# Optimization experiments

Measured on AMD Instinct MI355X. Metric: run time of the kernel, lower is better.

## Reference

```python
import jax, jax.numpy as jnp
import numpy as np

N = 50000   # nodes (= node_input)
H = 128     # node_hidden
E = 800000  # edges per adjacency


def spmm(row, col, val, dense):
    # (sparse NxN) @ dense[N, F] via gather + segment_sum
    return jax.ops.segment_sum(dense[col] * val[:, None], row, num_segments=N)


def l2norm(x, eps=1e-12):
    n = jnp.sqrt(jnp.sum(x * x, axis=1, keepdims=True))
    return x / jnp.maximum(n, eps)


def setup_inputs() -> dict:
    key = jax.random.key(0)
    ks = jax.random.split(key, 20)
    stdv = 1.0 / np.sqrt(H)
    u = lambda k, shape, s: jax.random.uniform(k, shape, jnp.float32, -s, s)
    inp = {
        'in_row': jax.random.randint(ks[0], (E,), 0, N),
        'in_col': jax.random.randint(ks[1], (E,), 0, N),
        'in_val': jax.random.uniform(ks[2], (E,), jnp.float32),
        'out_row': jax.random.randint(ks[3], (E,), 0, N),
        'out_col': jax.random.randint(ks[4], (E,), 0, N),
        'out_val': jax.random.uniform(ks[5], (E,), jnp.float32),
        'W1': u(ks[6], (N, H), stdv), 'b1': u(ks[7], (H,), stdv),
        'W2': u(ks[8], (H, H), stdv), 'b2': u(ks[9], (H,), stdv),
        'W3': u(ks[10], (H, H), stdv), 'b3': u(ks[11], (H,), stdv),
        'W4': u(ks[12], (H, H), stdv), 'b4': u(ks[13], (H,), stdv),
        'lin1_w': jax.random.normal(ks[14], (2 * H, H), jnp.float32) * 0.05,
        'lin1_b': jnp.zeros((2 * H,), jnp.float32),
        'lin2_w': jax.random.normal(ks[15], (2 * H, 2 * H), jnp.float32) * 0.05,
        'lin2_b': jnp.zeros((2 * H,), jnp.float32),
        'lin3_w': jax.random.normal(ks[16], (1, 2 * H), jnp.float32) * 0.05,
        'lin3_b': jnp.zeros((1,), jnp.float32),
    }
    return inp


def reference(in_row, in_col, in_val, out_row, out_col, out_val,
              W1, b1, W2, b2, W3, b3, W4, b4,
              lin1_w, lin1_b, lin2_w, lin2_b, lin3_w, lin3_b):
    def branch(row, col, val):
        x1 = l2norm(jax.nn.relu(spmm(row, col, val, W1) + b1))
        x2 = l2norm(jax.nn.relu(spmm(row, col, val, x1 @ W2) + b2))
        x3 = l2norm(jax.nn.relu(spmm(row, col, val, x2 @ W3) + b3))
        x4 = jax.nn.relu(spmm(row, col, val, x3 @ W4) + b4)
        return (x1, x2, x3, x4)

    def score(x):  # dropout p=0.0 -> identity
        h = jax.nn.relu(x @ lin1_w.T + lin1_b)
        h = jax.nn.relu(h @ lin2_w.T + lin2_b)
        return h @ lin3_w.T + lin3_b

    xs_in = branch(in_row, in_col, in_val)
    xs_out = branch(out_row, out_col, out_val)
    score_in = sum(score(x) for x in xs_in)
    score_out = sum(score(x) for x in xs_out)
    return score_in * score_out
```

## Files before the change

### kernel.cpp

```cpp
#include <hip/hip_runtime.h>
#include <hip/hip_bf16.h>

#define NN 50000
#define HH 128
#define H2 256
#define EE 800000
#define NBUCK 196
#define BINCH 4096
#define QB 128

typedef _Float16 half8 __attribute__((ext_vector_type(8)));
typedef float float4v __attribute__((ext_vector_type(4)));

__device__ __forceinline__ float bf2f(unsigned short u) {
  union { unsigned int i; float f; } v; v.i = ((unsigned int)u) << 16; return v.f;
}
__device__ __forceinline__ unsigned short f2bf(float f) {
  union { float f; unsigned int i; } v; v.f = f;
  unsigned int x = v.i;
  unsigned int r = x + 0x7fffu + ((x >> 16) & 1u);
  return (unsigned short)(r >> 16);
}

__device__ __forceinline__ unsigned int uenc(float x) {
  unsigned int b = (unsigned int)(x * 255.f + 0.5f);
  return b > 255u ? 255u : b;
}

__device__ __forceinline__ void udec(unsigned int wd, float vs, float* a) {
  a[0] = fmaf(vs, (float)(wd & 0xffu), a[0]);
  a[1] = fmaf(vs, (float)((wd >> 8) & 0xffu), a[1]);
  a[2] = fmaf(vs, (float)((wd >> 16) & 0xffu), a[2]);
  a[3] = fmaf(vs, (float)(wd >> 24), a[3]);
}

__global__ void detect_kernel(const unsigned int* __restrict__ val, int* __restrict__ dt) {
  unsigned int w = val[threadIdx.x];
  unsigned short u = (unsigned short)(w & 0xffff);
  int expf = (u >> 7) & 0xff;
  bool match = ((u >> 15) == 0) && expf >= 0x5A && expf <= 0x7E;
  unsigned long long m = __ballot(match);
  if (threadIdx.x == 0) dt[0] = (__popcll(m) >= 48) ? 1 : 0;
}

#define NSEG 14
struct ConvSegs {
  const void* s[NSEG];
  void* d[NSEG];
  int n[NSEG];
  int mode[NSEG];
  int kd[NSEG];
  int bstart[NSEG + 1];
};

__global__ __launch_bounds__(256) void convall_kernel(ConvSegs cs, const int* __restrict__ dt) {
  int b = blockIdx.x;
  int seg = 0;
  while (b >= cs.bstart[seg + 1]) ++seg;
  int i = (b - cs.bstart[seg]) * 256 + threadIdx.x;
  if (i >= cs.n[seg]) return;
  float f = dt[0] ? bf2f(((const unsigned short*)cs.s[seg])[i])
                  : ((const float*)cs.s[seg])[i];
  int m = cs.mode[seg];
  if (m == 0) { ((float*)cs.d[seg])[i] = f; return; }
  if (m == 1) { ((_Float16*)cs.d[seg])[i] = (_Float16)f; return; }
  int K = cs.kd[seg];
  int n, k;
  if (m == 3) { n = i / K; k = i - n * K; }
  else        { k = i >> 7; n = i & 127; }
  int NC16 = (cs.n[seg] / K) >> 4;
  int off = ((k >> 5) * NC16 + (n >> 4)) * 512 + (((k >> 3) & 3) * 16 + (n & 15)) * 8 + (k & 7);
  ((_Float16*)cs.d[seg])[off] = (_Float16)f;
}

__global__ __launch_bounds__(256) void bincount_kernel(
    const int* __restrict__ r0, const int* __restrict__ r1,
    int* __restrict__ bcnt, int E) {
  int br = blockIdx.y;
  const int* rows = br ? r1 : r0;
  __shared__ int cnt_s[NBUCK];
  int t = threadIdx.x;
  for (int i = t; i < NBUCK; i += 256) cnt_s[i] = 0;
  __syncthreads();
  int e0 = blockIdx.x * BINCH;
  #pragma unroll
  for (int i = 0; i < 16; ++i) {
    int e = e0 + i * 256 + t;
    if (e < E) atomicAdd(&cnt_s[rows[e] >> 8], 1);
  }
  __syncthreads();
  for (int i = t; i < NBUCK; i += 256) {
    int c = cnt_s[i];
    if (c) atomicAdd(&bcnt[br * NBUCK + i], c);
  }
}

__global__ __launch_bounds__(256) void bscan_kernel(const int* __restrict__ bcnt,
                                                    int* __restrict__ bbase,
                                                    int* __restrict__ gcur) {
  int br = blockIdx.y, t = threadIdx.x;
  __shared__ int s[256];
  int v = (t < NBUCK) ? bcnt[br * NBUCK + t] : 0;
  s[t] = v;
  __syncthreads();
  for (int off = 1; off < 256; off <<= 1) {
    int u = (t >= off) ? s[t - off] : 0;
    __syncthreads();
    s[t] += u;
    __syncthreads();
  }
  int ex = s[t] - v;
  if (t < NBUCK) { bbase[br * NBUCK + t] = ex; gcur[br * NBUCK + t] = ex; }
}

__global__ __launch_bounds__(256) void bin_kernel(
    const int* __restrict__ r0, const int* __restrict__ r1,
    const int* __restrict__ c0, const int* __restrict__ c1,
    const void* __restrict__ v0, const void* __restrict__ v1,
    int* __restrict__ gcur, int2* __restrict__ binned, int E, const int* __restrict__ dt) {
  int br = blockIdx.y;
  const int* rows = br ? r1 : r0;
  const int* cols = br ? c1 : c0;
  const void* vals = br ? v1 : v0;
  int2* bout = binned + (size_t)br * EE;
  int* cur = gcur + br * NBUCK;
  __shared__ int cnt_s[NBUCK];
  __shared__ int base_s[NBUCK];
  int t = threadIdx.x;
  for (int i = t; i < NBUCK; i += 256) cnt_s[i] = 0;
  __syncthreads();
  int e0 = blockIdx.x * BINCH;
  int row[16], col[16], vb[16];
  int cnt = 0;
  bool isb = dt[0] != 0;
  #pragma unroll
  for (int i = 0; i < 16; ++i) {
    int e = e0 + i * 256 + t;
    if (e < E) {
      row[cnt] = rows[e];
      col[cnt] = cols[e];
      float v = isb ? bf2f(((const unsigned short*)vals)[e]) : ((const float*)vals)[e];
      vb[cnt] = __float_as_int(v);
      atomicAdd(&cnt_s[row[cnt] >> 8], 1);
      ++cnt;
    }
  }
  __syncthreads();
  for (int i = t; i < NBUCK; i += 256) {
    int c = cnt_s[i];
    base_s[i] = c ? atomicAdd(&cur[i], c) : 0;
    cnt_s[i] = 0;
  }
  __syncthreads();
  for (int i = 0; i < cnt; ++i) {
    int b = row[i] >> 8;
    int off = atomicAdd(&cnt_s[b], 1);
    bout[base_s[b] + off] = make_int2((row[i] << 16) | col[i], vb[i]);
  }
}

__global__ __launch_bounds__(256) void bucket_kernel(
    const int* __restrict__ bbase, const int2* __restrict__ binned,
    int2* __restrict__ edges, int* __restrict__ rp, int N, int E) {
  int br = blockIdx.y, b = blockIdx.x, t = threadIdx.x;
  const int2* bin = binned + (size_t)br * EE;
  int2* eo = edges + (size_t)br * EE;
  int* r = rp + br * (NN + 1);
  __shared__ int cur[256];
  __shared__ int s[256];
  int base = bbase[br * NBUCK + b];
  int end  = (b + 1 < NBUCK) ? bbase[br * NBUCK + b + 1] : E;
  cur[t] = 0;
  __syncthreads();
  for (int i = base + t; i < end; i += 256)
    atomicAdd(&cur[(((unsigned)bin[i].x) >> 16) & 255], 1);
  __syncthreads();
  int v = cur[t];
  s[t] = v;
  __syncthreads();
  for (int off = 1; off < 256; off <<= 1) {
    int u = (t >= off) ? s[t - off] : 0;
    __syncthreads();
    s[t] += u;
    __syncthreads();
  }
  int ex = base + s[t] - v;
  int row = b * 256 + t;
  if (row < N) r[row] = ex;
  if (b == 0 && t == 0) r[N] = E;
  cur[t] = ex;
  __syncthreads();
  for (int i = base + t; i < end; i += 256) {
    int2 e = bin[i];
    int rl = (((unsigned)e.x) >> 16) & 255;
    int p = atomicAdd(&cur[rl], 1);
    eo[p] = make_int2(e.x & 0xffff, e.y);
  }
}

template<int DO_L2, int SQ>
__global__ __launch_bounds__(256) void spmm_kernel(
    const int* __restrict__ rp, const int2* __restrict__ edges,
    const _Float16* __restrict__ src, size_t sstride, const float* __restrict__ bias,
    _Float16* __restrict__ dst, size_t dstride, unsigned char* __restrict__ dstq, int N)
{
  const size_t XQC = (size_t)(NN + 128) * QB;
  int br = blockIdx.y;
  rp += br * (NN + 1);
  edges += (size_t)br * EE;
  src += br * sstride;
  dst += br * dstride;
  if (SQ) dstq += br * XQC;
  int g = threadIdx.x >> 4;
  int l = threadIdx.x & 15;
  int r = blockIdx.x * 16 + g;
  if (r >= N) return;
  int kb = rp[r], ke = rp[r + 1];
  float a0[8] = {0,0,0,0,0,0,0,0}, a1[8] = {0,0,0,0,0,0,0,0};
  float a2[8] = {0,0,0,0,0,0,0,0}, a3[8] = {0,0,0,0,0,0,0,0};
  int k = kb;
  for (; k + 3 < ke; k += 4) {
    int2 e0 = edges[k], e1 = edges[k + 1], e2 = edges[k + 2], e3 = edges[k + 3];
    half8 s0 = *(const half8*)(src + (size_t)e0.x * HH + l * 8);
    half8 s1 = *(const half8*)(src + (size_t)e1.x * HH + l * 8);
    half8 s2 = *(const half8*)(src + (size_t)e2.x * HH + l * 8);
    half8 s3 = *(const half8*)(src + (size_t)e3.x * HH + l * 8);
    float v0 = __int_as_float(e0.y), v1 = __int_as_float(e1.y);
    float v2 = __int_as_float(e2.y), v3 = __int_as_float(e3.y);
    #pragma unroll
    for (int j = 0; j < 8; ++j) {
      a0[j] = fmaf(v0, (float)s0[j], a0[j]);
      a1[j] = fmaf(v1, (float)s1[j], a1[j]);
      a2[j] = fmaf(v2, (float)s2[j], a2[j]);
      a3[j] = fmaf(v3, (float)s3[j], a3[j]);
    }
  }
  for (; k < ke; ++k) {
    int2 e0 = edges[k];
    half8 s0 = *(const half8*)(src + (size_t)e0.x * HH + l * 8);
    float v0 = __int_as_float(e0.y);
    #pragma unroll
    for (int j = 0; j < 8; ++j) a0[j] = fmaf(v0, (float)s0[j], a0[j]);
  }
  float x[8];
  #pragma unroll
  for (int j = 0; j < 8; ++j)
    x[j] = fmaxf((a0[j] + a1[j]) + (a2[j] + a3[j]) + bias[l * 8 + j], 0.f);
  if (DO_L2) {
    float ss = 0.f;
    #pragma unroll
    for (int j = 0; j < 8; ++j) ss += x[j] * x[j];
    #pragma unroll
    for (int m = 1; m < 16; m <<= 1) ss += __shfl_xor(ss, m, 64);
    float sc = 1.f / fmaxf(sqrtf(ss), 1e-12f);
    #pragma unroll
    for (int j = 0; j < 8; ++j) x[j] *= sc;
  }
  half8 hv;
  #pragma unroll
  for (int j = 0; j < 8; ++j) hv[j] = (_Float16)x[j];
  *(half8*)&dst[(size_t)r * HH + l * 8] = hv;
  if (SQ) {
    uint2 qo;
    qo.x = uenc(x[0]) | (uenc(x[1]) << 8) | (uenc(x[2]) << 16) | (uenc(x[3]) << 24);
    qo.y = uenc(x[4]) | (uenc(x[5]) << 8) | (uenc(x[6]) << 16) | (uenc(x[7]) << 24);
    *(uint2*)(dstq + (size_t)r * QB + l * 8) = qo;
  }
}

template<int DO_L2, int GQ, int SQ>
__global__ __launch_bounds__(256, 6) void fused_kernel(
    const int* __restrict__ rp, const int2* __restrict__ edges,
    const _Float16* __restrict__ xcur, const unsigned char* __restrict__ xq,
    _Float16* __restrict__ xnext, unsigned char* __restrict__ xnq,
    const _Float16* __restrict__ wt, const float* __restrict__ bias,
    const _Float16* __restrict__ w1, const _Float16* __restrict__ w2,
    const float* __restrict__ b1v, const float* __restrict__ b2v,
    const float* __restrict__ w3v,
    float* __restrict__ S, int N, int sg, int gx, int nsp)
{
  extern __shared__ _Float16 smem[];
  const size_t XSC = (size_t)(NN + 128) * HH;
  const size_t XQC = (size_t)(NN + 128) * QB;
  int br = blockIdx.y;
  rp += br * (NN + 1);
  edges += (size_t)br * EE;
  xcur += br * XSC;
  if (GQ) xq += br * XQC;

  int bx = blockIdx.x;
  int role, idx;
  if (nsp) {
    int q = bx / 3, k3 = bx - q * 3;
    if (k3 < 2) { idx = q * 2 + k3; if (idx >= sg) return; role = 0; }
    else        { idx = q;          if (idx >= gx) return; role = 1; }
  } else { role = 1; idx = bx; if (idx >= gx) return; }

  const int lane = threadIdx.x & 63, w = threadIdx.x >> 6;
  const int lm = lane & 15, lq = lane >> 4;

  if (role == 0) {
    xnext += br * XSC;
    if (SQ) xnq += br * XQC;
    int g = threadIdx.x >> 4, l = threadIdx.x & 15;
    int r = idx * 16 + g;
    int kb = rp[r], ke = rp[r + 1];
    half8 hv;
    float a0[8] = {0,0,0,0,0,0,0,0}, a1[8] = {0,0,0,0,0,0,0,0};
    float a2[8] = {0,0,0,0,0,0,0,0}, a3[8] = {0,0,0,0,0,0,0,0};
    if (GQ) {
      int k = kb;
      for (; k + 3 < ke; k += 4) {
        int2 e0 = edges[k], e1 = edges[k + 1], e2 = edges[k + 2], e3 = edges[k + 3];
        uint2 q0 = *(const uint2*)(xq + (size_t)e0.x * QB + l * 8);
        uint2 q1 = *(const uint2*)(xq + (size_t)e1.x * QB + l * 8);
        uint2 q2 = *(const uint2*)(xq + (size_t)e2.x * QB + l * 8);
        uint2 q3 = *(const uint2*)(xq + (size_t)e3.x * QB + l * 8);
        float v0 = __int_as_float(e0.y) * (1.f / 255.f);
        float v1 = __int_as_float(e1.y) * (1.f / 255.f);
        float v2 = __int_as_float(e2.y) * (1.f / 255.f);
        float v3 = __int_as_float(e3.y) * (1.f / 255.f);
        udec(q0.x, v0, a0); udec(q0.y, v0, a0 + 4);
        udec(q1.x, v1, a1); udec(q1.y, v1, a1 + 4);
        udec(q2.x, v2, a2); udec(q2.y, v2, a2 + 4);
        udec(q3.x, v3, a3); udec(q3.y, v3, a3 + 4);
      }
      for (; k < ke; ++k) {
        int2 e0 = edges[k];
        uint2 q0 = *(const uint2*)(xq + (size_t)e0.x * QB + l * 8);
        float v0 = __int_as_float(e0.y) * (1.f / 255.f);
        udec(q0.x, v0, a0); udec(q0.y, v0, a0 + 4);
      }
    } else {
      int k = kb;
      for (; k + 3 < ke; k += 4) {
        int2 e0 = edges[k], e1 = edges[k + 1], e2 = edges[k + 2], e3 = edges[k + 3];
        half8 s0 = *(const half8*)(xcur + (size_t)e0.x * HH + l * 8);
        half8 s1 = *(const half8*)(xcur + (size_t)e1.x * HH + l * 8);
        half8 s2 = *(const half8*)(xcur + (size_t)e2.x * HH + l * 8);
        half8 s3 = *(const half8*)(xcur + (size_t)e3.x * HH + l * 8);
        float v0 = __int_as_float(e0.y), v1 = __int_as_float(e1.y);
        float v2 = __int_as_float(e2.y), v3 = __int_as_float(e3.y);
        #pragma unroll
        for (int j = 0; j < 8; ++j) {
          a0[j] = fmaf(v0, (float)s0[j], a0[j]);
          a1[j] = fmaf(v1, (float)s1[j], a1[j]);
          a2[j] = fmaf(v2, (float)s2[j], a2[j]);
          a3[j] = fmaf(v3, (float)s3[j], a3[j]);
        }
      }
      for (; k < ke; ++k) {
        int2 e0 = edges[k];
        half8 s0 = *(const half8*)(xcur + (size_t)e0.x * HH + l * 8);
        float v0 = __int_as_float(e0.y);
        #pragma unroll
        for (int j = 0; j < 8; ++j) a0[j] = fmaf(v0, (float)s0[j], a0[j]);
      }
    }
    #pragma unroll
    for (int j = 0; j < 8; ++j)
      hv[j] = (_Float16)((a0[j] + a1[j]) + (a2[j] + a3[j]));
    *(half8*)&smem[g * 136 + l * 8] = hv;
    __syncthreads();

    float4v acc[2];
    acc[0] = (float4v){0.f,0.f,0.f,0.f};
    acc[1] = (float4v){0.f,0.f,0.f,0.f};
    #pragma unroll
    for (int k0 = 0; k0 < HH; k0 += 32) {
      half8 ah = *(const half8*)&smem[lm * 136 + k0 + lq * 8];
      #pragma unroll
      for (int nt = 0; nt < 2; ++nt) {
        half8 bh = *(const half8*)(wt + (((k0 >> 5) * 8) + w * 2 + nt) * 512 + lane * 8);
        acc[nt] = __builtin_amdgcn_mfma_f32_16x16x32_f16(ah, bh, acc[nt], 0, 0, 0);
      }
    }
    float v[2][4];
    float ssp[4] = {0.f, 0.f, 0.f, 0.f};
    #pragma unroll
    for (int nt = 0; nt < 2; ++nt) {
      float bv = bias[w * 32 + nt * 16 + lm];
      #pragma unroll
      for (int rr = 0; rr < 4; ++rr) {
        float t = fmaxf(acc[nt][rr] + bv, 0.f);
        v[nt][rr] = t;
        ssp[rr] += t * t;
      }
    }
    if (DO_L2) {
      #pragma unroll
      for (int m = 1; m < 16; m <<= 1) {
        #pragma unroll
        for (int rr = 0; rr < 4; ++rr) ssp[rr] += __shfl_xor(ssp[rr], m, 64);
      }
      float* sred = (float*)(smem + 16 * 136);
      if (lm == 0) {
        #pragma unroll
        for (int rr = 0; rr < 4; ++rr) sred[w * 16 + lq * 4 + rr] = ssp[rr];
      }
      __syncthreads();
      #pragma unroll
      for (int rr = 0; rr < 4; ++rr) {
        int rowl = lq * 4 + rr;
        float tot = sred[rowl] + sred[16 + rowl] + sred[32 + rowl] + sred[48 + rowl];
        float sc = 1.f / fmaxf(sqrtf(tot), 1e-12f);
        v[0][rr] *= sc;
        v[1][rr] *= sc;
      }
    }
    #pragma unroll
    for (int rr = 0; rr < 4; ++rr) {
      size_t ro = (size_t)(idx * 16 + lq * 4 + rr) * HH;
      #pragma unroll
      for (int nt = 0; nt < 2; ++nt)
        xnext[ro + w * 32 + nt * 16 + lm] = (_Float16)v[nt][rr];
    }
    if (SQ) {
      __syncthreads();
      #pragma unroll
      for (int rr = 0; rr < 4; ++rr) {
        int rowl = lq * 4 + rr;
        #pragma unroll
        for (int nt = 0; nt < 2; ++nt)
          smem[rowl * 136 + w * 32 + nt * 16 + lm] = (_Float16)v[nt][rr];
      }
      __syncthreads();
      unsigned int bq[8];
      #pragma unroll
      for (int j = 0; j < 8; ++j)
        bq[j] = uenc((float)smem[g * 136 + l * 8 + j]);
      uint2 qo;
      qo.x = bq[0] | (bq[1] << 8) | (bq[2] << 16) | (bq[3] << 24);
      qo.y = bq[4] | (bq[5] << 8) | (bq[6] << 16) | (bq[7] << 24);
      *(uint2*)(xnq + (size_t)r * QB + l * 8) = qo;
    }
    return;
  }

  float* Sb = S + (size_t)br * N;
  _Float16* h1s = smem;
  const int HS = H2 + 8;
  const int m0 = idx * 32;
  const int wn = w * 64;
  {
    float4v acc[2][4];
    #pragma unroll
    for (int i = 0; i < 2; ++i)
      #pragma unroll
      for (int j = 0; j < 4; ++j) acc[i][j] = (float4v){0.f,0.f,0.f,0.f};
    #pragma unroll
    for (int k0 = 0; k0 < HH; k0 += 32) {
      half8 ah[2], bh[4];
      #pragma unroll
      for (int mt = 0; mt < 2; ++mt)
        ah[mt] = *(const half8*)(xcur + (size_t)(m0 + mt * 16 + lm) * HH + k0 + lq * 8);
      #pragma unroll
      for (int nt = 0; nt < 4; ++nt)
        bh[nt] = *(const half8*)(w1 + (((k0 >> 5) * 16) + (wn >> 4) + nt) * 512 + lane * 8);
      #pragma unroll
      for (int mt = 0; mt < 2; ++mt)
        #pragma unroll
        for (int nt = 0; nt < 4; ++nt)
          acc[mt][nt] = __builtin_amdgcn_mfma_f32_16x16x32_f16(ah[mt], bh[nt], acc[mt][nt], 0, 0, 0);
    }
    float bv[4];
    #pragma unroll
    for (int nt = 0; nt < 4; ++nt) bv[nt] = b1v[wn + nt * 16 + lm];
    #pragma unroll
    for (int mt = 0; mt < 2; ++mt)
      #pragma unroll
      for (int rr = 0; rr < 4; ++rr) {
        int rowl = mt * 16 + lq * 4 + rr;
        #pragma unroll
        for (int nt = 0; nt < 4; ++nt)
          h1s[rowl * HS + wn + nt * 16 + lm] = (_Float16)fmaxf(acc[mt][nt][rr] + bv[nt], 0.f);
      }
  }
  __syncthreads();
  {
    float4v acc[2][4];
    #pragma unroll
    for (int i = 0; i < 2; ++i)
      #pragma unroll
      for (int j = 0; j < 4; ++j) acc[i][j] = (float4v){0.f,0.f,0.f,0.f};
    #pragma unroll
    for (int k0 = 0; k0 < H2; k0 += 32) {
      half8 ah[2], bh[4];
      #pragma unroll
      for (int mt = 0; mt < 2; ++mt)
        ah[mt] = *(const half8*)&h1s[(mt * 16 + lm) * HS + k0 + lq * 8];
      #pragma unroll
      for (int nt = 0; nt < 4; ++nt)
        bh[nt] = *(const half8*)(w2 + (((k0 >> 5) * 16) + (wn >> 4) + nt) * 512 + lane * 8);
      #pragma unroll
      for (int mt = 0; mt < 2; ++mt)
        #pragma unroll
        for (int nt = 0; nt < 4; ++nt)
          acc[mt][nt] = __builtin_amdgcn_mfma_f32_16x16x32_f16(ah[mt], bh[nt], acc[mt][nt], 0, 0, 0);
    }
    float bv[4], wv[4];
    #pragma unroll
    for (int nt = 0; nt < 4; ++nt) {
      int col = wn + nt * 16 + lm;
      bv[nt] = b2v[col]; wv[nt] = w3v[col];
    }
    #pragma unroll
    for (int mt = 0; mt < 2; ++mt)
      #pragma unroll
      for (int rr = 0; rr < 4; ++rr) {
        float p = 0.f;
        #pragma unroll
        for (int nt = 0; nt < 4; ++nt)
          p += fmaxf(acc[mt][nt][rr] + bv[nt], 0.f) * wv[nt];
        p += __shfl_xor(p, 1, 64);
        p += __shfl_xor(p, 2, 64);
        p += __shfl_xor(p, 4, 64);
        p += __shfl_xor(p, 8, 64);
        if (lm == 0) {
          int row = m0 + mt * 16 + lq * 4 + rr;
          if (row < N) atomicAdd(&Sb[row], p);
        }
      }
  }
}

__global__ void final_kernel(const float* __restrict__ s_in, const float* __restrict__ s_out,
                             const float* __restrict__ b3, void* __restrict__ out, int N,
                             const int* __restrict__ dt) {
  int i = blockIdx.x * 256 + threadIdx.x;
  if (i >= N) return;
  float b = 4.f * b3[0];
  float v = (s_in[i] + b) * (s_out[i] + b);
  if (dt[0]) ((unsigned short*)out)[i] = f2bf(v);
  else       ((float*)out)[i] = v;
}

extern "C" void kernel_launch(void* const* d_in, const int* in_sizes, int n_in,
                              void* d_out, int out_size, void* d_ws, size_t ws_size,
                              hipStream_t stream) {
  const int N = NN, E = EE;

  char* ws = (char*)d_ws;
  size_t o = 0;
  auto alloc = [&](size_t bytes) -> void* {
    void* p = ws + o;
    o = (o + bytes + 255) & ~(size_t)255;
    return p;
  };

  int* dt = (int*)alloc(16);
  float* bc[4]; float* l1b; float* l2b; float* w3f; float* l3b;
  for (int i = 0; i < 4; ++i) bc[i] = (float*)alloc(HH * 4);
  l1b = (float*)alloc(H2 * 4);
  l2b = (float*)alloc(H2 * 4);
  w3f = (float*)alloc(H2 * 4);
  l3b = (float*)alloc(4);
  _Float16* l1w_h = (_Float16*)alloc(H2 * HH * 2);
  _Float16* l2w_h = (_Float16*)alloc(H2 * H2 * 2);
  _Float16* Wt_h[3];
  for (int i = 0; i < 3; ++i) Wt_h[i] = (_Float16*)alloc(HH * HH * 2);
  _Float16* w1_h = (_Float16*)alloc((size_t)N * HH * 2);

  const int NP = N + 128;
  const size_t XS = (size_t)NP * HH;
  const size_t XQ = (size_t)NP * QB;
  int* rp    = (int*)alloc(2 * (size_t)(N + 1) * 4);
  int* bcnt  = (int*)alloc(2 * NBUCK * 4);
  int* bbase = (int*)alloc(2 * NBUCK * 4);
  int* gcur  = (int*)alloc(2 * NBUCK * 4);
  int2* binned = (int2*)alloc(2 * (size_t)E * 8);
  int2* edges  = (int2*)alloc(2 * (size_t)E * 8);
  _Float16* x_h  = (_Float16*)alloc(2 * XS * 2);
  _Float16* tb_h = (_Float16*)alloc(2 * XS * 2);
  unsigned char* x_q  = (unsigned char*)alloc(2 * XQ);
  unsigned char* tb_q = (unsigned char*)alloc(2 * XQ);
  float* sacc = (float*)alloc(2 * (size_t)N * 4);

  dim3 blk(256);
  detect_kernel<<<1, 64, 0, stream>>>((const unsigned int*)d_in[2], dt);

  ConvSegs cs;
  const void* srcs[NSEG] = {d_in[7], d_in[9], d_in[11], d_in[13], d_in[15], d_in[17],
                            d_in[18], d_in[19], d_in[14], d_in[16], d_in[8], d_in[10],
                            d_in[12], d_in[6]};
  void* dsts[NSEG] = {bc[0], bc[1], bc[2], bc[3], l1b, l2b, w3f, l3b,
                      l1w_h, l2w_h, Wt_h[0], Wt_h[1], Wt_h[2], w1_h};
  int ns[NSEG] = {HH, HH, HH, HH, H2, H2, H2, 1,
                  H2 * HH, H2 * H2, HH * HH, HH * HH, HH * HH, N * HH};
  int ms[NSEG] = {0, 0, 0, 0, 0, 0, 0, 0, 3, 3, 4, 4, 4, 1};
  int ks[NSEG] = {0, 0, 0, 0, 0, 0, 0, 0, HH, H2, HH, HH, HH, 0};
  int btot = 0;
  for (int i = 0; i < NSEG; ++i) {
    cs.s[i] = srcs[i]; cs.d[i] = dsts[i]; cs.n[i] = ns[i]; cs.mode[i] = ms[i]; cs.kd[i] = ks[i];
    cs.bstart[i] = btot;
    btot += (ns[i] + 255) / 256;
  }
  cs.bstart[NSEG] = btot;
  convall_kernel<<<btot, blk, 0, stream>>>(cs, dt);

  hipMemsetAsync(sacc, 0, 2 * (size_t)N * 4, stream);
  hipMemsetAsync(bcnt, 0, 2 * NBUCK * 4, stream);
  hipMemsetAsync(x_h  + (size_t)N * HH, 0, (size_t)128 * HH * 2, stream);
  hipMemsetAsync(x_h  + XS + (size_t)N * HH, 0, (size_t)128 * HH * 2, stream);
  hipMemsetAsync(tb_h + (size_t)N * HH, 0, (size_t)128 * HH * 2, stream);
  hipMemsetAsync(tb_h + XS + (size_t)N * HH, 0, (size_t)128 * HH * 2, stream);

  int sg   = (N + 15) / 16;
  int gx32 = (N + 31) / 32;
  int mg   = ((sg + 1) / 2) * 3;
  int bg   = (E + BINCH - 1) / BINCH;
  const size_t FLDS = (size_t)32 * (H2 + 8) * sizeof(_Float16);

  bincount_kernel<<<dim3(bg, 2), blk, 0, stream>>>((const int*)d_in[0], (const int*)d_in[3], bcnt, E);
  bscan_kernel<<<dim3(1, 2), blk, 0, stream>>>(bcnt, bbase, gcur);
  bin_kernel<<<dim3(bg, 2), blk, 0, stream>>>(
      (const int*)d_in[0], (const int*)d_in[3], (const int*)d_in[1], (const int*)d_in[4],
      d_in[2], d_in[5], gcur, binned, E, dt);
  bucket_kernel<<<dim3(NBUCK, 2), blk, 0, stream>>>(bbase, binned, edges, rp, N, E);

  spmm_kernel<1, 1><<<dim3(sg, 2), blk, 0, stream>>>(rp, edges, w1_h, 0, bc[0], x_h, XS, x_q, N);

  fused_kernel<1, 1, 1><<<dim3(mg, 2), blk, FLDS, stream>>>(
      rp, edges, x_h, x_q, tb_h, tb_q, Wt_h[0], bc[1], l1w_h, l2w_h, l1b, l2b, w3f,
      sacc, N, sg, gx32, 1);
  fused_kernel<1, 1, 1><<<dim3(mg, 2), blk, FLDS, stream>>>(
      rp, edges, tb_h, tb_q, x_h, x_q, Wt_h[1], bc[2], l1w_h, l2w_h, l1b, l2b, w3f,
      sacc, N, sg, gx32, 1);
  fused_kernel<0, 1, 0><<<dim3(mg, 2), blk, FLDS, stream>>>(
      rp, edges, x_h, x_q, tb_h, nullptr, Wt_h[2], bc[3], l1w_h, l2w_h, l1b, l2b, w3f,
      sacc, N, sg, gx32, 1);
  fused_kernel<0, 0, 0><<<dim3(gx32, 2), blk, FLDS, stream>>>(
      rp, edges, tb_h, nullptr, nullptr, nullptr, nullptr, nullptr, l1w_h, l2w_h, l1b, l2b, w3f,
      sacc, N, 0, gx32, 0);

  final_kernel<<<(N + 255) / 256, blk, 0, stream>>>(sacc, sacc + N, l3b, d_out, N, dt);
}
```

Before: 545.0 us.

## Process 32 rows per SpMM block with 16-byte quantized gathers and coalesced stores

The SpMM role of the fused kernel now handles 32 rows per block instead of 16. Eight threads cover each row and gather 16 quantized bytes per edge instead of 8. The MFMA step computes a 32x128 tile with two M-subtiles, and the output goes through shared memory so fp16 and uint8 rows are written in wide coalesced stores. The grid interleaves SpMM and score blocks 1:1 instead of 2:1, and the now-unused non-quantized gather path is removed. This trades fewer, wider memory transactions and better weight reuse against fewer threads per row and more registers per thread, which may reduce latency hiding on the irregular gathers.

```diff
diff --git a/kernel.cpp b/kernel.cpp
--- a/kernel.cpp
+++ b/kernel.cpp
@@ -26,7 +26,6 @@
   unsigned int b = (unsigned int)(x * 255.f + 0.5f);
   return b > 255u ? 255u : b;
 }
-
 __device__ __forceinline__ void udec(unsigned int wd, float vs, float* a) {
   a[0] = fmaf(vs, (float)(wd & 0xffu), a[0]);
   a[1] = fmaf(vs, (float)((wd >> 8) & 0xffu), a[1]);
@@ -268,7 +267,7 @@
   }
 }
 
-template<int DO_L2, int GQ, int SQ>
+template<int DO_L2, int SQ>
 __global__ __launch_bounds__(256, 6) void fused_kernel(
     const int* __restrict__ rp, const int2* __restrict__ edges,
     const _Float16* __restrict__ xcur, const unsigned char* __restrict__ xq,
@@ -286,153 +285,154 @@
   rp += br * (NN + 1);
   edges += (size_t)br * EE;
   xcur += br * XSC;
-  if (GQ) xq += br * XQC;
 
   int bx = blockIdx.x;
   int role, idx;
   if (nsp) {
-    int q = bx / 3, k3 = bx - q * 3;
-    if (k3 < 2) { idx = q * 2 + k3; if (idx >= sg) return; role = 0; }
-    else        { idx = q;          if (idx >= gx) return; role = 1; }
+    idx = bx >> 1;
+    if (bx & 1) { role = 1; if (idx >= gx) return; }
+    else        { role = 0; if (idx >= sg) return; }
   } else { role = 1; idx = bx; if (idx >= gx) return; }
 
   const int lane = threadIdx.x & 63, w = threadIdx.x >> 6;
   const int lm = lane & 15, lq = lane >> 4;
 
   if (role == 0) {
-    xnext += br * XSC;
-    if (SQ) xnq += br * XQC;
-    int g = threadIdx.x >> 4, l = threadIdx.x & 15;
-    int r = idx * 16 + g;
-    int kb = rp[r], ke = rp[r + 1];
-    half8 hv;
-    float a0[8] = {0,0,0,0,0,0,0,0}, a1[8] = {0,0,0,0,0,0,0,0};
-    float a2[8] = {0,0,0,0,0,0,0,0}, a3[8] = {0,0,0,0,0,0,0,0};
-    if (GQ) {
-      int k = kb;
-      for (; k + 3 < ke; k += 4) {
-        int2 e0 = edges[k], e1 = edges[k + 1], e2 = edges[k + 2], e3 = edges[k + 3];
-        uint2 q0 = *(const uint2*)(xq + (size_t)e0.x * QB + l * 8);
-        uint2 q1 = *(const uint2*)(xq + (size_t)e1.x * QB + l * 8);
-        uint2 q2 = *(const uint2*)(xq + (size_t)e2.x * QB + l * 8);
-        uint2 q3 = *(const uint2*)(xq + (size_t)e3.x * QB + l * 8);
-        float v0 = __int_as_float(e0.y) * (1.f / 255.f);
-        float v1 = __int_as_float(e1.y) * (1.f / 255.f);
-        float v2 = __int_as_float(e2.y) * (1.f / 255.f);
-        float v3 = __int_as_float(e3.y) * (1.f / 255.f);
-        udec(q0.x, v0, a0); udec(q0.y, v0, a0 + 4);
-        udec(q1.x, v1, a1); udec(q1.y, v1, a1 + 4);
-        udec(q2.x, v2, a2); udec(q2.y, v2, a2 + 4);
-        udec(q3.x, v3, a3); udec(q3.y, v3, a3 + 4);
-      }
-      for (; k < ke; ++k) {
-        int2 e0 = edges[k];
-        uint2 q0 = *(const uint2*)(xq + (size_t)e0.x * QB + l * 8);
-        float v0 = __int_as_float(e0.y) * (1.f / 255.f);
-        udec(q0.x, v0, a0); udec(q0.y, v0, a0 + 4);
-      }
-    } else {
-      int k = kb;
-      for (; k + 3 < ke; k += 4) {
-        int2 e0 = edges[k], e1 = edges[k + 1], e2 = edges[k + 2], e3 = edges[k + 3];
-        half8 s0 = *(const half8*)(xcur + (size_t)e0.x * HH + l * 8);
-        half8 s1 = *(const half8*)(xcur + (size_t)e1.x * HH + l * 8);
-        half8 s2 = *(const half8*)(xcur + (size_t)e2.x * HH + l * 8);
-        half8 s3 = *(const half8*)(xcur + (size_t)e3.x * HH + l * 8);
-        float v0 = __int_as_float(e0.y), v1 = __int_as_float(e1.y);
-        float v2 = __int_as_float(e2.y), v3 = __int_as_float(e3.y);
-        #pragma unroll
-        for (int j = 0; j < 8; ++j) {
-          a0[j] = fmaf(v0, (float)s0[j], a0[j]);
-          a1[j] = fmaf(v1, (float)s1[j], a1[j]);
-          a2[j] = fmaf(v2, (float)s2[j], a2[j]);
-          a3[j] = fmaf(v3, (float)s3[j], a3[j]);
-        }
-      }
-      for (; k < ke; ++k) {
-        int2 e0 = edges[k];
-        half8 s0 = *(const half8*)(xcur + (size_t)e0.x * HH + l * 8);
-        float v0 = __int_as_float(e0.y);
-        #pragma unroll
-        for (int j = 0; j < 8; ++j) a0[j] = fmaf(v0, (float)s0[j], a0[j]);
-      }
-    }
-    #pragma unroll
-    for (int j = 0; j < 8; ++j)
-      hv[j] = (_Float16)((a0[j] + a1[j]) + (a2[j] + a3[j]));
-    *(half8*)&smem[g * 136 + l * 8] = hv;
+    const unsigned char* xqb = xq + br * XQC;
+    _Float16* xnb = xnext + br * XSC;
+    unsigned char* xnqb = SQ ? (xnq + br * XQC) : nullptr;
+    int g = threadIdx.x >> 3, l = threadIdx.x & 7;
+    int r = idx * 32 + g;
+    int kb = 0, ke = 0;
+    if (r < N) { kb = rp[r]; ke = rp[r + 1]; }
+    float a[16];
+    #pragma unroll
+    for (int j = 0; j < 16; ++j) a[j] = 0.f;
+    int k = kb;
+    for (; k + 3 < ke; k += 4) {
+      int2 e0 = edges[k], e1 = edges[k + 1], e2 = edges[k + 2], e3 = edges[k + 3];
+      uint4 q0 = *(const uint4*)(xqb + (size_t)e0.x * QB + l * 16);
+      uint4 q1 = *(const uint4*)(xqb + (size_t)e1.x * QB + l * 16);
+      uint4 q2 = *(const uint4*)(xqb + (size_t)e2.x * QB + l * 16);
+      uint4 q3 = *(const uint4*)(xqb + (size_t)e3.x * QB + l * 16);
+      float v0 = __int_as_float(e0.y) * (1.f / 255.f);
+      float v1 = __int_as_float(e1.y) * (1.f / 255.f);
+      float v2 = __int_as_float(e2.y) * (1.f / 255.f);
+      float v3 = __int_as_float(e3.y) * (1.f / 255.f);
+      udec(q0.x, v0, a); udec(q0.y, v0, a + 4); udec(q0.z, v0, a + 8); udec(q0.w, v0, a + 12);
+      udec(q1.x, v1, a); udec(q1.y, v1, a + 4); udec(q1.z, v1, a + 8); udec(q1.w, v1, a + 12);
+      udec(q2.x, v2, a); udec(q2.y, v2, a + 4); udec(q2.z, v2, a + 8); udec(q2.w, v2, a + 12);
+      udec(q3.x, v3, a); udec(q3.y, v3, a + 4); udec(q3.z, v3, a + 8); udec(q3.w, v3, a + 12);
+    }
+    for (; k < ke; ++k) {
+      int2 e0 = edges[k];
+      uint4 q0 = *(const uint4*)(xqb + (size_t)e0.x * QB + l * 16);
+      float v0 = __int_as_float(e0.y) * (1.f / 255.f);
+      udec(q0.x, v0, a); udec(q0.y, v0, a + 4); udec(q0.z, v0, a + 8); udec(q0.w, v0, a + 12);
+    }
+    {
+      half8 h0, h1;
+      #pragma unroll
+      for (int j = 0; j < 8; ++j) { h0[j] = (_Float16)a[j]; h1[j] = (_Float16)a[j + 8]; }
+      *(half8*)&smem[g * 136 + l * 16] = h0;
+      *(half8*)&smem[g * 136 + l * 16 + 8] = h1;
+    }
     __syncthreads();
 
-    float4v acc[2];
-    acc[0] = (float4v){0.f,0.f,0.f,0.f};
-    acc[1] = (float4v){0.f,0.f,0.f,0.f};
+    float4v acc[2][2];
+    #pragma unroll
+    for (int i = 0; i < 2; ++i)
+      #pragma unroll
+      for (int j = 0; j < 2; ++j) acc[i][j] = (float4v){0.f, 0.f, 0.f, 0.f};
     #pragma unroll
     for (int k0 = 0; k0 < HH; k0 += 32) {
-      half8 ah = *(const half8*)&smem[lm * 136 + k0 + lq * 8];
-      #pragma unroll
-      for (int nt = 0; nt < 2; ++nt) {
-        half8 bh = *(const half8*)(wt + (((k0 >> 5) * 8) + w * 2 + nt) * 512 + lane * 8);
-        acc[nt] = __builtin_amdgcn_mfma_f32_16x16x32_f16(ah, bh, acc[nt], 0, 0, 0);
-      }
-    }
-    float v[2][4];
-    float ssp[4] = {0.f, 0.f, 0.f, 0.f};
+      half8 ah[2], bh[2];
+      #pragma unroll
+      for (int mt = 0; mt < 2; ++mt)
+        ah[mt] = *(const half8*)&smem[(mt * 16 + lm) * 136 + k0 + lq * 8];
+      #pragma unroll
+      for (int nt = 0; nt < 2; ++nt)
+        bh[nt] = *(const half8*)(wt + (((k0 >> 5) * 8) + w * 2 + nt) * 512 + lane * 8);
+      #pragma unroll
+      for (int mt = 0; mt < 2; ++mt)
+        #pragma unroll
+        for (int nt = 0; nt < 2; ++nt)
+          acc[mt][nt] = __builtin_amdgcn_mfma_f32_16x16x32_f16(ah[mt], bh[nt], acc[mt][nt], 0, 0, 0);
+    }
+    float vv[2][2][4];
+    float ssp[2][4];
+    #pragma unroll
+    for (int mt = 0; mt < 2; ++mt)
+      #pragma unroll
+      for (int rr = 0; rr < 4; ++rr) ssp[mt][rr] = 0.f;
     #pragma unroll
     for (int nt = 0; nt < 2; ++nt) {
       float bv = bias[w * 32 + nt * 16 + lm];
       #pragma unroll
+      for (int mt = 0; mt < 2; ++mt)
+        #pragma unroll
+        for (int rr = 0; rr < 4; ++rr) {
+          float t = fmaxf(acc[mt][nt][rr] + bv, 0.f);
+          vv[mt][nt][rr] = t;
+          ssp[mt][rr] += t * t;
+        }
+    }
+    if (DO_L2) {
+      #pragma unroll
+      for (int m = 1; m < 16; m <<= 1)
+        #pragma unroll
+        for (int mt = 0; mt < 2; ++mt)
+          #pragma unroll
+          for (int rr = 0; rr < 4; ++rr) ssp[mt][rr] += __shfl_xor(ssp[mt][rr], m, 64);
+      float* sred = (float*)(smem + 32 * 136);
+      if (lm == 0)
+        #pragma unroll
+        for (int mt = 0; mt < 2; ++mt)
+          #pragma unroll
+          for (int rr = 0; rr < 4; ++rr) sred[w * 32 + mt * 16 + lq * 4 + rr] = ssp[mt][rr];
+      __syncthreads();
+      #pragma unroll
+      for (int mt = 0; mt < 2; ++mt)
+        #pragma unroll
+        for (int rr = 0; rr < 4; ++rr) {
+          int rowl = mt * 16 + lq * 4 + rr;
+          float tot = sred[rowl] + sred[32 + rowl] + sred[64 + rowl] + sred[96 + rowl];
+          float sc = 1.f / fmaxf(sqrtf(tot), 1e-12f);
+          vv[mt][0][rr] *= sc;
+          vv[mt][1][rr] *= sc;
+        }
+    } else {
+      __syncthreads();
+    }
+    #pragma unroll
+    for (int mt = 0; mt < 2; ++mt)
+      #pragma unroll
       for (int rr = 0; rr < 4; ++rr) {
-        float t = fmaxf(acc[nt][rr] + bv, 0.f);
-        v[nt][rr] = t;
-        ssp[rr] += t * t;
+        int rowl = mt * 16 + lq * 4 + rr;
+        #pragma unroll
+        for (int nt = 0; nt < 2; ++nt)
+          smem[rowl * 136 + w * 32 + nt * 16 + lm] = (_Float16)vv[mt][nt][rr];
       }
-    }
-    if (DO_L2) {
-      #pragma unroll
-      for (int m = 1; m < 16; m <<= 1) {
-        #pragma unroll
-        for (int rr = 0; rr < 4; ++rr) ssp[rr] += __shfl_xor(ssp[rr], m, 64);
+    __syncthreads();
+    if (r < N) {
+      half8 h0 = *(const half8*)&smem[g * 136 + l * 16];
+      half8 h1 = *(const half8*)&smem[g * 136 + l * 16 + 8];
+      *(half8*)&xnb[(size_t)r * HH + l * 16] = h0;
+      *(half8*)&xnb[(size_t)r * HH + l * 16 + 8] = h1;
+      if (SQ) {
+        unsigned int bq[16];
+        #pragma unroll
+        for (int j = 0; j < 8; ++j) {
+          bq[j] = uenc((float)h0[j]);
+          bq[8 + j] = uenc((float)h1[j]);
+        }
+        uint4 qo;
+        qo.x = bq[0]  | (bq[1] << 8)  | (bq[2] << 16)  | (bq[3] << 24);
+        qo.y = bq[4]  | (bq[5] << 8)  | (bq[6] << 16)  | (bq[7] << 24);
+        qo.z = bq[8]  | (bq[9] << 8)  | (bq[10] << 16) | (bq[11] << 24);
+        qo.w = bq[12] | (bq[13] << 8) | (bq[14] << 16) | (bq[15] << 24);
+        *(uint4*)(xnqb + (size_t)r * QB + l * 16) = qo;
       }
-      float* sred = (float*)(smem + 16 * 136);
-      if (lm == 0) {
-        #pragma unroll
-        for (int rr = 0; rr < 4; ++rr) sred[w * 16 + lq * 4 + rr] = ssp[rr];
-      }
-      __syncthreads();
-      #pragma unroll
-      for (int rr = 0; rr < 4; ++rr) {
-        int rowl = lq * 4 + rr;
-        float tot = sred[rowl] + sred[16 + rowl] + sred[32 + rowl] + sred[48 + rowl];
-        float sc = 1.f / fmaxf(sqrtf(tot), 1e-12f);
-        v[0][rr] *= sc;
-        v[1][rr] *= sc;
-      }
-    }
-    #pragma unroll
-    for (int rr = 0; rr < 4; ++rr) {
-      size_t ro = (size_t)(idx * 16 + lq * 4 + rr) * HH;
-      #pragma unroll
-      for (int nt = 0; nt < 2; ++nt)
-        xnext[ro + w * 32 + nt * 16 + lm] = (_Float16)v[nt][rr];
-    }
-    if (SQ) {
-      __syncthreads();
-      #pragma unroll
-      for (int rr = 0; rr < 4; ++rr) {
-        int rowl = lq * 4 + rr;
-        #pragma unroll
-        for (int nt = 0; nt < 2; ++nt)
-          smem[rowl * 136 + w * 32 + nt * 16 + lm] = (_Float16)v[nt][rr];
-      }
-      __syncthreads();
-      unsigned int bq[8];
-      #pragma unroll
-      for (int j = 0; j < 8; ++j)
-        bq[j] = uenc((float)smem[g * 136 + l * 8 + j]);
-      uint2 qo;
-      qo.x = bq[0] | (bq[1] << 8) | (bq[2] << 16) | (bq[3] << 24);
-      qo.y = bq[4] | (bq[5] << 8) | (bq[6] << 16) | (bq[7] << 24);
-      *(uint2*)(xnq + (size_t)r * QB + l * 8) = qo;
     }
     return;
   }
@@ -606,8 +606,9 @@
   hipMemsetAsync(tb_h + XS + (size_t)N * HH, 0, (size_t)128 * HH * 2, stream);
 
   int sg   = (N + 15) / 16;
+  int sg32 = (N + 31) / 32;
   int gx32 = (N + 31) / 32;
-  int mg   = ((sg + 1) / 2) * 3;
+  int mg   = 2 * sg32;
   int bg   = (E + BINCH - 1) / BINCH;
   const size_t FLDS = (size_t)32 * (H2 + 8) * sizeof(_Float16);
 
@@ -620,16 +621,16 @@
 
   spmm_kernel<1, 1><<<dim3(sg, 2), blk, 0, stream>>>(rp, edges, w1_h, 0, bc[0], x_h, XS, x_q, N);
 
-  fused_kernel<1, 1, 1><<<dim3(mg, 2), blk, FLDS, stream>>>(
+  fused_kernel<1, 1><<<dim3(mg, 2), blk, FLDS, stream>>>(
       rp, edges, x_h, x_q, tb_h, tb_q, Wt_h[0], bc[1], l1w_h, l2w_h, l1b, l2b, w3f,
-      sacc, N, sg, gx32, 1);
-  fused_kernel<1, 1, 1><<<dim3(mg, 2), blk, FLDS, stream>>>(
+      sacc, N, sg32, gx32, 1);
+  fused_kernel<1, 1><<<dim3(mg, 2), blk, FLDS, stream>>>(
       rp, edges, tb_h, tb_q, x_h, x_q, Wt_h[1], bc[2], l1w_h, l2w_h, l1b, l2b, w3f,
-      sacc, N, sg, gx32, 1);
-  fused_kernel<0, 1, 0><<<dim3(mg, 2), blk, FLDS, stream>>>(
+      sacc, N, sg32, gx32, 1);
+  fused_kernel<0, 0><<<dim3(mg, 2), blk, FLDS, stream>>>(
       rp, edges, x_h, x_q, tb_h, nullptr, Wt_h[2], bc[3], l1w_h, l2w_h, l1b, l2b, w3f,
-      sacc, N, sg, gx32, 1);
-  fused_kernel<0, 0, 0><<<dim3(gx32, 2), blk, FLDS, stream>>>(
+      sacc, N, sg32, gx32, 1);
+  fused_kernel<0, 0><<<dim3(gx32, 2), blk, FLDS, stream>>>(
       rp, edges, tb_h, nullptr, nullptr, nullptr, nullptr, nullptr, l1w_h, l2w_h, l1b, l2b, w3f,
       sacc, N, 0, gx32, 0);
 
```

Result: no change. 539.2 us (-1.1%).
